# Optimization experiments

Hardware: AMD Instinct MI355X
Metric: run time of the kernel (lower is better)

The kernel has to match this reference:

```python
import jax, jax.numpy as jnp
import numpy as np

N = 8192
K = 8192
BS = 128  # quantization block size (elements per codebook)
NE = 8    # codebook entries per block (3-bit indices)


def setup_inputs() -> dict:
    key = jax.random.key(0)
    k1, k2, k3 = jax.random.split(key, 3)
    num_blocks = N * K // BS  # 524288
    n_packed_bytes = num_blocks * BS * 3 // 8  # 25165824
    x = jax.random.normal(k1, (2048, K), dtype=jnp.float32)
    # random packed bytes (values 0..255) -> uniformly random 3-bit indices
    packed_indices = jax.random.randint(k2, (n_packed_bytes,), 0, 256, dtype=jnp.int32)
    codebook = jax.random.normal(k3, (num_blocks, NE), dtype=jnp.float32)
    return {"x": x, "packed_indices": packed_indices, "codebook": codebook}


def _dequantize(packed_indices, codebook):
    num_blocks = codebook.shape[0]
    packed = packed_indices.reshape(-1, 3).astype(jnp.int32)  # (n_groups, 3)
    bits24 = packed[:, 0] | (packed[:, 1] << 8) | (packed[:, 2] << 16)
    shifts = jnp.arange(8, dtype=jnp.int32) * 3
    idx = (bits24[:, None] >> shifts[None, :]) & 7          # (n_groups, 8)
    idx = idx.reshape(num_blocks, BS)                        # (num_blocks, BS)
    # per-block codebook gather: w[b, i] = codebook[b, idx[b, i]]
    w = jnp.take_along_axis(codebook, idx, axis=1)           # (num_blocks, BS)
    return w.reshape(N, K)


def reference(x, packed_indices, codebook):
    w = _dequantize(packed_indices, codebook)  # (N, K) fp32
    y = x @ w.T                                # (batch, N)
    return y
```

## Files before the change

kernel.cpp:

```cpp
#include <hip/hip_runtime.h>
#include <hip/hip_bf16.h>

#define Mdim 2048
#define Ndim 8192
#define Kdim 8192
#define BM 128
#define BN 128
#define BK 64

typedef __bf16 bf16x8 __attribute__((ext_vector_type(8)));
typedef float f32x4 __attribute__((ext_vector_type(4)));
typedef unsigned short ushort8 __attribute__((ext_vector_type(8)));
typedef unsigned short ushort4v __attribute__((ext_vector_type(4)));

__device__ __forceinline__ unsigned short f2bf_rne(float f) {
    unsigned u = __float_as_uint(f);
    u += 0x7fffu + ((u >> 16) & 1u);
    return (unsigned short)(u >> 16);
}

__device__ __forceinline__ ushort8 decode8(unsigned bits, float4 c0, float4 c1) {
    ushort8 o;
#pragma unroll
    for (int i = 0; i < 8; ++i) {
        unsigned id = (bits >> (3 * i)) & 7u;
        float a0 = (id & 1) ? c0.y : c0.x;
        float a1 = (id & 1) ? c0.w : c0.z;
        float a2 = (id & 1) ? c1.y : c1.x;
        float a3 = (id & 1) ? c1.w : c1.z;
        float b0 = (id & 2) ? a1 : a0;
        float b1 = (id & 2) ? a3 : a2;
        float v  = (id & 4) ? b1 : b0;
        o[i] = f2bf_rne(v);
    }
    return o;
}

__global__ __launch_bounds__(256) void k_prep(const int* __restrict__ packed,
                                              const float* __restrict__ cb,
                                              const float* __restrict__ x,
                                              unsigned short* __restrict__ W,
                                              unsigned short* __restrict__ xb) {
    const int t = threadIdx.x;
    if (blockIdx.x < 16384) {
        const size_t th = (size_t)blockIdx.x * 256 + t;
        const size_t g0 = th * 2;
        const int2* pv = (const int2*)(packed + g0 * 3);
        int2 q0 = pv[0], q1 = pv[1], q2 = pv[2];
        unsigned bits0 = (unsigned)(q0.x & 255) | ((unsigned)(q0.y & 255) << 8) |
                         ((unsigned)(q1.x & 255) << 16);
        unsigned bits1 = (unsigned)(q1.y & 255) | ((unsigned)(q2.x & 255) << 8) |
                         ((unsigned)(q2.y & 255) << 16);
        const float4* cv0 = (const float4*)(cb + ((g0 >> 4) << 3));
        const float4* cv1 = (const float4*)(cb + (((g0 + 1) >> 4) << 3));
        float4 c00 = cv0[0], c01 = cv0[1];
        float4 c10 = cv1[0], c11 = cv1[1];
        ushort8 o0 = decode8(bits0, c00, c01);
        ushort8 o1 = decode8(bits1, c10, c11);
        unsigned short* wp = W + (g0 << 3);
        *(ushort8*)(wp)     = o0;
        *(ushort8*)(wp + 8) = o1;
    } else {
        const size_t u = (size_t)(blockIdx.x - 16384) * 256 + t;
        float4 a = ((const float4*)x)[u];
        ushort4v o;
        o[0] = f2bf_rne(a.x); o[1] = f2bf_rne(a.y);
        o[2] = f2bf_rne(a.z); o[3] = f2bf_rne(a.w);
        ((ushort4v*)xb)[u] = o;
    }
}

__device__ __forceinline__ void gld16(const unsigned short* g, unsigned short* l) {
    __builtin_amdgcn_global_load_lds(
        (const __attribute__((address_space(1))) unsigned int*)g,
        (__attribute__((address_space(3))) unsigned int*)l, 16, 0, 0);
}

__global__ __launch_bounds__(256) void k_gemm(const unsigned short* __restrict__ A,
                                              const unsigned short* __restrict__ B,
                                              float* __restrict__ C) {
    __shared__ unsigned short As[BM * BK];
    __shared__ unsigned short Bs[BN * BK];

    const int tid  = threadIdx.x;
    const int lane = tid & 63;
    const int wave = tid >> 6;
    const int waveM = wave >> 1;
    const int waveN = wave & 1;
    const int bm = blockIdx.y * BM;
    const int bn = blockIdx.x * BN;

    const int srow = tid >> 3;
    const int scol = (((tid & 7) ^ ((tid >> 3) & 7))) * 8;
    const unsigned short* agp = A + (size_t)(bm + srow) * Kdim + scol;
    const unsigned short* bgp = B + (size_t)(bn + srow) * Kdim + scol;
    unsigned short* alp = &As[tid * 8];
    unsigned short* blp = &Bs[tid * 8];

    f32x4 acc[4][4];
    const f32x4 zero = {0.f, 0.f, 0.f, 0.f};
#pragma unroll
    for (int i = 0; i < 4; ++i)
#pragma unroll
        for (int j = 0; j < 4; ++j) acc[i][j] = zero;

    const int r15 = lane & 15;
    const int q   = lane >> 4;
    const int rlo = r15 & 7;

    for (int kt = 0; kt < Kdim; kt += BK) {
#pragma unroll
        for (int j = 0; j < 4; ++j) {
            gld16(agp + (size_t)(j * 32) * Kdim + kt, alp + j * 2048);
            gld16(bgp + (size_t)(j * 32) * Kdim + kt, blp + j * 2048);
        }
        __syncthreads();

#pragma unroll
        for (int kk = 0; kk < 2; ++kk) {
            const int slot = ((kk * 4 + q) ^ rlo) * 8;
            bf16x8 af[4], bfr[4];
#pragma unroll
            for (int i = 0; i < 4; ++i)
                af[i] = *(const bf16x8*)(&As[(waveM * 64 + i * 16 + r15) * BK + slot]);
#pragma unroll
            for (int j = 0; j < 4; ++j)
                bfr[j] = *(const bf16x8*)(&Bs[(waveN * 64 + j * 16 + r15) * BK + slot]);
#pragma unroll
            for (int i = 0; i < 4; ++i)
#pragma unroll
                for (int j = 0; j < 4; ++j)
                    acc[i][j] = __builtin_amdgcn_mfma_f32_16x16x32_bf16(
                        af[i], bfr[j], acc[i][j], 0, 0, 0);
        }
        __syncthreads();
    }

#pragma unroll
    for (int i = 0; i < 4; ++i) {
#pragma unroll
        for (int j = 0; j < 4; ++j) {
            int row = bm + waveM * 64 + i * 16 + q * 4;
            int col = bn + waveN * 64 + j * 16 + r15;
            float* outp = C + (size_t)row * Ndim + col;
#pragma unroll
            for (int r = 0; r < 4; ++r)
                outp[(size_t)r * Ndim] = acc[i][j][r];
        }
    }
}

extern "C" void kernel_launch(void* const* d_in, const int* in_sizes, int n_in,
                              void* d_out, int out_size, void* d_ws, size_t ws_size,
                              hipStream_t stream) {
    const float* x      = (const float*)d_in[0];
    const int*   packed = (const int*)d_in[1];
    const float* cb     = (const float*)d_in[2];
    float* out = (float*)d_out;

    unsigned short* Wb = (unsigned short*)d_ws;
    unsigned short* Xb = (unsigned short*)d_ws + (size_t)Ndim * Kdim;

    k_prep<<<32768, 256, 0, stream>>>(packed, cb, x, Wb, Xb);
    dim3 grid(Ndim / BN, Mdim / BM);
    k_gemm<<<grid, 256, 0, stream>>>(Xb, Wb, out);
}
```

Before: 525.0 us.

## Rewrite GEMM as 256x256 tile, 8-wave, double-buffered pipelined kernel

Replaces the 128x128 single-buffered GEMM with a 256x256 output tile per 512-thread block. The block computes four 128x128 quadrants in phases and uses a double-buffered LDS ring. Global-to-LDS loads for the next k-tiles are issued between MFMA phases, with explicit vmcnt waits, raw barriers and setprio, to overlap memory with compute and raise reuse per loaded byte. This adds heavy register pressure (128 accumulator floats plus fragments), 128KB of LDS, and fragile hand-tuned barrier and waitcnt ordering.

Result: faster. 473.0 us (-9.9%).

```diff
diff --git a/kernel.cpp b/kernel.cpp
--- a/kernel.cpp
+++ b/kernel.cpp
@@ -4,9 +4,7 @@
 #define Mdim 2048
 #define Ndim 8192
 #define Kdim 8192
-#define BM 128
-#define BN 128
-#define BK 64
+#define NT (Kdim / 64)
 
 typedef __bf16 bf16x8 __attribute__((ext_vector_type(8)));
 typedef float f32x4 __attribute__((ext_vector_type(4)));
@@ -76,78 +74,155 @@
         (__attribute__((address_space(3))) unsigned int*)l, 16, 0, 0);
 }
 
-__global__ __launch_bounds__(256) void k_gemm(const unsigned short* __restrict__ A,
-                                              const unsigned short* __restrict__ B,
-                                              float* __restrict__ C) {
-    __shared__ unsigned short As[BM * BK];
-    __shared__ unsigned short Bs[BN * BK];
+#define BAR()    asm volatile("s_barrier" ::: "memory")
+#define FENCE()  asm volatile("" ::: "memory")
+#define WAIT_DS0() asm volatile("s_waitcnt lgkmcnt(0)" ::: "memory")
+
+__global__ __launch_bounds__(512, 2) void k_gemm(const unsigned short* __restrict__ A,
+                                                 const unsigned short* __restrict__ B,
+                                                 float* __restrict__ C) {
+    __shared__ unsigned short LA[4 * 8192];
+    __shared__ unsigned short LB[4 * 8192];
 
     const int tid  = threadIdx.x;
     const int lane = tid & 63;
     const int wave = tid >> 6;
-    const int waveM = wave >> 1;
-    const int waveN = wave & 1;
-    const int bm = blockIdx.y * BM;
-    const int bn = blockIdx.x * BN;
-
-    const int srow = tid >> 3;
-    const int scol = (((tid & 7) ^ ((tid >> 3) & 7))) * 8;
-    const unsigned short* agp = A + (size_t)(bm + srow) * Kdim + scol;
-    const unsigned short* bgp = B + (size_t)(bn + srow) * Kdim + scol;
-    unsigned short* alp = &As[tid * 8];
-    unsigned short* blp = &Bs[tid * 8];
-
-    f32x4 acc[4][4];
-    const f32x4 zero = {0.f, 0.f, 0.f, 0.f};
-#pragma unroll
-    for (int i = 0; i < 4; ++i)
-#pragma unroll
-        for (int j = 0; j < 4; ++j) acc[i][j] = zero;
+    const int qm = wave >> 2;
+    const int qn = wave & 3;
+
+    const int bid = blockIdx.x;
+    const int bm = (bid & 7) * 256;
+    const int bn = (bid >> 3) * 256;
+
+    const int chunk0 = tid, chunk1 = tid + 512;
+    const int srow0 = chunk0 >> 3, srow1 = chunk1 >> 3;
+    const int scol0 = ((chunk0 & 7) ^ (srow0 & 7)) * 8;
+    const int scol1 = ((chunk1 & 7) ^ (srow1 & 7)) * 8;
+    const unsigned short* Ag0 = A + (size_t)(bm + srow0) * Kdim + scol0;
+    const unsigned short* Ag1 = A + (size_t)(bm + srow1) * Kdim + scol1;
+    const unsigned short* Bg0 = B + (size_t)(bn + srow0) * Kdim + scol0;
+    const unsigned short* Bg1 = B + (size_t)(bn + srow1) * Kdim + scol1;
+
+#define STAGE_A(T, H, BUF) do {                                                   \
+    unsigned short* _d = LA + ((BUF) * 2 + (H)) * 8192;                           \
+    gld16(Ag0 + (size_t)(H) * 128 * Kdim + (size_t)(T) * 64, _d + (size_t)tid * 8);        \
+    gld16(Ag1 + (size_t)(H) * 128 * Kdim + (size_t)(T) * 64, _d + (size_t)(tid + 512) * 8);\
+    FENCE();                                                                      \
+} while (0)
+#define STAGE_B(T, H, BUF) do {                                                   \
+    unsigned short* _d = LB + ((BUF) * 2 + (H)) * 8192;                           \
+    gld16(Bg0 + (size_t)(H) * 128 * Kdim + (size_t)(T) * 64, _d + (size_t)tid * 8);        \
+    gld16(Bg1 + (size_t)(H) * 128 * Kdim + (size_t)(T) * 64, _d + (size_t)(tid + 512) * 8);\
+    FENCE();                                                                      \
+} while (0)
 
     const int r15 = lane & 15;
     const int q   = lane >> 4;
     const int rlo = r15 & 7;
-
-    for (int kt = 0; kt < Kdim; kt += BK) {
-#pragma unroll
-        for (int j = 0; j < 4; ++j) {
-            gld16(agp + (size_t)(j * 32) * Kdim + kt, alp + j * 2048);
-            gld16(bgp + (size_t)(j * 32) * Kdim + kt, blp + j * 2048);
+    const int aro = qm * 64 + r15;
+    const int bro = qn * 32 + r15;
+    const int ch0 = ((0 + q) ^ rlo) * 8;
+    const int ch1 = ((4 + q) ^ rlo) * 8;
+
+    f32x4 acc[4][4][2];
+    const f32x4 zero = {0.f, 0.f, 0.f, 0.f};
+#pragma unroll
+    for (int p = 0; p < 4; ++p)
+#pragma unroll
+        for (int i = 0; i < 4; ++i)
+#pragma unroll
+            for (int j = 0; j < 2; ++j) acc[p][i][j] = zero;
+
+    bf16x8 af[4][2], bf[2][2];
+
+#define LOAD_A(BUF, H) do {                                                       \
+    const unsigned short* _s = LA + ((BUF) * 2 + (H)) * 8192;                     \
+    _Pragma("unroll") for (int i = 0; i < 4; ++i) {                               \
+        int _r = (aro + i * 16) * 64;                                             \
+        af[i][0] = *(const bf16x8*)&_s[_r + ch0];                                 \
+        af[i][1] = *(const bf16x8*)&_s[_r + ch1];                                 \
+    }                                                                             \
+} while (0)
+#define LOAD_B(BUF, H) do {                                                       \
+    const unsigned short* _s = LB + ((BUF) * 2 + (H)) * 8192;                     \
+    _Pragma("unroll") for (int j = 0; j < 2; ++j) {                               \
+        int _r = (bro + j * 16) * 64;                                             \
+        bf[j][0] = *(const bf16x8*)&_s[_r + ch0];                                 \
+        bf[j][1] = *(const bf16x8*)&_s[_r + ch1];                                 \
+    }                                                                             \
+} while (0)
+
+#define MFMA_PHASE(P) do {                                                        \
+    __builtin_amdgcn_s_setprio(1);                                                \
+    _Pragma("unroll") for (int i = 0; i < 4; ++i)                                 \
+    _Pragma("unroll") for (int j = 0; j < 2; ++j) {                               \
+        acc[P][i][j] = __builtin_amdgcn_mfma_f32_16x16x32_bf16(                   \
+            af[i][0], bf[j][0], acc[P][i][j], 0, 0, 0);                           \
+        acc[P][i][j] = __builtin_amdgcn_mfma_f32_16x16x32_bf16(                   \
+            af[i][1], bf[j][1], acc[P][i][j], 0, 0, 0);                           \
+    }                                                                             \
+    __builtin_amdgcn_s_setprio(0);                                                \
+} while (0)
+
+#define KSTEP(T, BUF) do {                                                        \
+    LOAD_A(BUF, 0); LOAD_B(BUF, 0);                                               \
+    if ((T) + 1 < NT) STAGE_B((T) + 1, 0, (BUF) ^ 1);                             \
+    BAR(); WAIT_DS0();                                                            \
+    MFMA_PHASE(0);                                                                \
+    BAR();                                                                        \
+    LOAD_B(BUF, 1);                                                               \
+    if ((T) + 2 < NT) STAGE_A((T) + 2, 0, BUF);                                   \
+    BAR(); WAIT_DS0();                                                            \
+    MFMA_PHASE(1);                                                                \
+    BAR();                                                                        \
+    LOAD_A(BUF, 1);                                                               \
+    if ((T) + 2 < NT) STAGE_B((T) + 2, 1, BUF);                                   \
+    BAR(); WAIT_DS0();                                                            \
+    MFMA_PHASE(2);                                                                \
+    BAR();                                                                        \
+    LOAD_B(BUF, 0);                                                               \
+    if ((T) + 2 < NT) STAGE_A((T) + 2, 1, BUF);                                   \
+    BAR(); WAIT_DS0();                                                            \
+    MFMA_PHASE(3);                                                                \
+    if ((T) + 2 < NT) { asm volatile("s_waitcnt vmcnt(6)" ::: "memory"); }        \
+    else              { asm volatile("s_waitcnt vmcnt(0)" ::: "memory"); }        \
+    BAR();                                                                        \
+} while (0)
+
+    STAGE_A(0, 0, 0); STAGE_B(0, 1, 0); STAGE_A(0, 1, 0); STAGE_B(0, 0, 0);
+    STAGE_A(1, 0, 1); STAGE_B(1, 1, 1); STAGE_A(1, 1, 1);
+    asm volatile("s_waitcnt vmcnt(6)" ::: "memory");
+    BAR();
+
+    for (int t2 = 0; t2 < NT; t2 += 2) {
+        KSTEP(t2, 0);
+        KSTEP(t2 + 1, 1);
+    }
+
+    constexpr int RHs[4] = {0, 0, 1, 1};
+    constexpr int CHs[4] = {0, 1, 1, 0};
+#pragma unroll
+    for (int p = 0; p < 4; ++p) {
+#pragma unroll
+        for (int i = 0; i < 4; ++i) {
+#pragma unroll
+            for (int j = 0; j < 2; ++j) {
+                int row = bm + RHs[p] * 128 + qm * 64 + i * 16 + q * 4;
+                int col = bn + CHs[p] * 128 + qn * 32 + j * 16 + r15;
+                float* outp = C + (size_t)row * Ndim + col;
+#pragma unroll
+                for (int r = 0; r < 4; ++r)
+                    outp[(size_t)r * Ndim] = acc[p][i][j][r];
+            }
         }
-        __syncthreads();
-
-#pragma unroll
-        for (int kk = 0; kk < 2; ++kk) {
-            const int slot = ((kk * 4 + q) ^ rlo) * 8;
-            bf16x8 af[4], bfr[4];
-#pragma unroll
-            for (int i = 0; i < 4; ++i)
-                af[i] = *(const bf16x8*)(&As[(waveM * 64 + i * 16 + r15) * BK + slot]);
-#pragma unroll
-            for (int j = 0; j < 4; ++j)
-                bfr[j] = *(const bf16x8*)(&Bs[(waveN * 64 + j * 16 + r15) * BK + slot]);
-#pragma unroll
-            for (int i = 0; i < 4; ++i)
-#pragma unroll
-                for (int j = 0; j < 4; ++j)
-                    acc[i][j] = __builtin_amdgcn_mfma_f32_16x16x32_bf16(
-                        af[i], bfr[j], acc[i][j], 0, 0, 0);
-        }
-        __syncthreads();
-    }
-
-#pragma unroll
-    for (int i = 0; i < 4; ++i) {
-#pragma unroll
-        for (int j = 0; j < 4; ++j) {
-            int row = bm + waveM * 64 + i * 16 + q * 4;
-            int col = bn + waveN * 64 + j * 16 + r15;
-            float* outp = C + (size_t)row * Ndim + col;
-#pragma unroll
-            for (int r = 0; r < 4; ++r)
-                outp[(size_t)r * Ndim] = acc[i][j][r];
-        }
-    }
+    }
+
+#undef STAGE_A
+#undef STAGE_B
+#undef LOAD_A
+#undef LOAD_B
+#undef MFMA_PHASE
+#undef KSTEP
 }
 
 extern "C" void kernel_launch(void* const* d_in, const int* in_sizes, int n_in,
@@ -162,6 +237,5 @@
     unsigned short* Xb = (unsigned short*)d_ws + (size_t)Ndim * Kdim;
 
     k_prep<<<32768, 256, 0, stream>>>(packed, cb, x, Wb, Xb);
-    dim3 grid(Ndim / BN, Mdim / BM);
-    k_gemm<<<grid, 256, 0, stream>>>(Xb, Wb, out);
-}
+    k_gemm<<<dim3(256), 512, 0, stream>>>(Xb, Wb, out);
+}
```

## Fuse codebook dequantization into GEMM with producer/consumer warp specialization

Applied to the files above, without the earlier changes.

Removes the separate pass that writes the full dequantized bf16 weight matrix to global memory. Dequantization now happens inside the GEMM: four producer waves load packed indices and codebooks, decode them into LDS with byte-perm selects, and stage A tiles. Four consumer waves run MFMA over a double-buffered 256x128 tile at raised priority. The goal is to cut the large weight write and re-read traffic. In exchange, W is decoded again for each of the 8 M-tiles and the kernel depends on hand-placed barrier and waitcnt synchronization.

New measurement: 678.1 us. 1.29x slower.

```diff
diff --git a/kernel.cpp b/kernel.cpp
--- a/kernel.cpp
+++ b/kernel.cpp
@@ -4,13 +4,12 @@
 #define Mdim 2048
 #define Ndim 8192
 #define Kdim 8192
-#define BM 128
+#define NT 128
+#define BM 256
 #define BN 128
-#define BK 64
 
 typedef __bf16 bf16x8 __attribute__((ext_vector_type(8)));
 typedef float f32x4 __attribute__((ext_vector_type(4)));
-typedef unsigned short ushort8 __attribute__((ext_vector_type(8)));
 typedef unsigned short ushort4v __attribute__((ext_vector_type(4)));
 
 __device__ __forceinline__ unsigned short f2bf_rne(float f) {
@@ -19,55 +18,14 @@
     return (unsigned short)(u >> 16);
 }
 
-__device__ __forceinline__ ushort8 decode8(unsigned bits, float4 c0, float4 c1) {
-    ushort8 o;
-#pragma unroll
-    for (int i = 0; i < 8; ++i) {
-        unsigned id = (bits >> (3 * i)) & 7u;
-        float a0 = (id & 1) ? c0.y : c0.x;
-        float a1 = (id & 1) ? c0.w : c0.z;
-        float a2 = (id & 1) ? c1.y : c1.x;
-        float a3 = (id & 1) ? c1.w : c1.z;
-        float b0 = (id & 2) ? a1 : a0;
-        float b1 = (id & 2) ? a3 : a2;
-        float v  = (id & 4) ? b1 : b0;
-        o[i] = f2bf_rne(v);
-    }
-    return o;
-}
-
-__global__ __launch_bounds__(256) void k_prep(const int* __restrict__ packed,
-                                              const float* __restrict__ cb,
-                                              const float* __restrict__ x,
-                                              unsigned short* __restrict__ W,
+__global__ __launch_bounds__(256) void k_prep(const float* __restrict__ x,
                                               unsigned short* __restrict__ xb) {
-    const int t = threadIdx.x;
-    if (blockIdx.x < 16384) {
-        const size_t th = (size_t)blockIdx.x * 256 + t;
-        const size_t g0 = th * 2;
-        const int2* pv = (const int2*)(packed + g0 * 3);
-        int2 q0 = pv[0], q1 = pv[1], q2 = pv[2];
-        unsigned bits0 = (unsigned)(q0.x & 255) | ((unsigned)(q0.y & 255) << 8) |
-                         ((unsigned)(q1.x & 255) << 16);
-        unsigned bits1 = (unsigned)(q1.y & 255) | ((unsigned)(q2.x & 255) << 8) |
-                         ((unsigned)(q2.y & 255) << 16);
-        const float4* cv0 = (const float4*)(cb + ((g0 >> 4) << 3));
-        const float4* cv1 = (const float4*)(cb + (((g0 + 1) >> 4) << 3));
-        float4 c00 = cv0[0], c01 = cv0[1];
-        float4 c10 = cv1[0], c11 = cv1[1];
-        ushort8 o0 = decode8(bits0, c00, c01);
-        ushort8 o1 = decode8(bits1, c10, c11);
-        unsigned short* wp = W + (g0 << 3);
-        *(ushort8*)(wp)     = o0;
-        *(ushort8*)(wp + 8) = o1;
-    } else {
-        const size_t u = (size_t)(blockIdx.x - 16384) * 256 + t;
-        float4 a = ((const float4*)x)[u];
-        ushort4v o;
-        o[0] = f2bf_rne(a.x); o[1] = f2bf_rne(a.y);
-        o[2] = f2bf_rne(a.z); o[3] = f2bf_rne(a.w);
-        ((ushort4v*)xb)[u] = o;
-    }
+    const size_t u = (size_t)blockIdx.x * 256 + threadIdx.x;
+    float4 a = ((const float4*)x)[u];
+    ushort4v o;
+    o[0] = f2bf_rne(a.x); o[1] = f2bf_rne(a.y);
+    o[2] = f2bf_rne(a.z); o[3] = f2bf_rne(a.w);
+    ((ushort4v*)xb)[u] = o;
 }
 
 __device__ __forceinline__ void gld16(const unsigned short* g, unsigned short* l) {
@@ -76,78 +34,204 @@
         (__attribute__((address_space(3))) unsigned int*)l, 16, 0, 0);
 }
 
-__global__ __launch_bounds__(256) void k_gemm(const unsigned short* __restrict__ A,
-                                              const unsigned short* __restrict__ B,
-                                              float* __restrict__ C) {
-    __shared__ unsigned short As[BM * BK];
-    __shared__ unsigned short Bs[BN * BK];
+#define BAR()    asm volatile("s_barrier" ::: "memory")
+#define FENCE()  asm volatile("" ::: "memory")
+#define LGKM0()  asm volatile("s_waitcnt lgkmcnt(0)" ::: "memory")
+#define VMCNT(n) asm volatile("s_waitcnt vmcnt(" #n ")" ::: "memory")
+
+__device__ __forceinline__ uint4 dec_group(unsigned b, unsigned P0, unsigned P1,
+                                           unsigned P2, unsigned P3) {
+    uint4 o;
+#pragma unroll
+    for (int k = 0; k < 4; ++k) {
+        unsigned ia = (b >> (6 * k)) & 3u;
+        unsigned ib = (b >> (6 * k + 3)) & 3u;
+        unsigned sel = ia * 0x0202u + 0x01000100u + ((ib * 0x0202u) << 16);
+        unsigned lo = __builtin_amdgcn_perm(P1, P0, sel);
+        unsigned hi = __builtin_amdgcn_perm(P3, P2, sel);
+        unsigned mA = (unsigned)((int)(b << (29 - 6 * k)) >> 31);
+        unsigned mB = (unsigned)((int)(b << (26 - 6 * k)) >> 31);
+        unsigned m = (mA & 0xFFFFu) | (mB & 0xFFFF0000u);
+        (&o.x)[k] = (hi & m) | (lo & ~m);
+    }
+    return o;
+}
+
+__global__ __launch_bounds__(512, 2) void k_gemm(const unsigned short* __restrict__ A,
+                                                 const int* __restrict__ packed,
+                                                 const float* __restrict__ cb,
+                                                 float* __restrict__ C) {
+    __shared__ unsigned short LA[2 * 16384];
+    __shared__ unsigned short LB[2 * 8192];
 
     const int tid  = threadIdx.x;
     const int lane = tid & 63;
     const int wave = tid >> 6;
-    const int waveM = wave >> 1;
-    const int waveN = wave & 1;
-    const int bm = blockIdx.y * BM;
-    const int bn = blockIdx.x * BN;
-
-    const int srow = tid >> 3;
-    const int scol = (((tid & 7) ^ ((tid >> 3) & 7))) * 8;
-    const unsigned short* agp = A + (size_t)(bm + srow) * Kdim + scol;
-    const unsigned short* bgp = B + (size_t)(bn + srow) * Kdim + scol;
-    unsigned short* alp = &As[tid * 8];
-    unsigned short* blp = &Bs[tid * 8];
-
-    f32x4 acc[4][4];
-    const f32x4 zero = {0.f, 0.f, 0.f, 0.f};
-#pragma unroll
-    for (int i = 0; i < 4; ++i)
-#pragma unroll
-        for (int j = 0; j < 4; ++j) acc[i][j] = zero;
+
+    const int bid = blockIdx.x;
+    const int bm = (bid & 7) * BM;
+    const int bn = (bid >> 3) * BN;
+
+    const int plane = (tid - 256) & 255;
+    const int arow0 = plane >> 3;
+    const int acol  = ((plane & 7) ^ (arow0 & 7)) * 8;
+    const unsigned short* Aga = A + (size_t)(bm + arow0) * Kdim + acol;
+
+    const int brow = plane >> 1;
+    const int dp   = plane & 1;
+    const int dp4  = dp * 4;
+    const int brlo = brow & 7;
+    const int* Pg   = packed + (size_t)(bn + brow) * 3072 + dp * 12;
+    const float* Cg = cb + (size_t)(bn + brow) * 512;
 
     const int r15 = lane & 15;
     const int q   = lane >> 4;
     const int rlo = r15 & 7;
-
-    for (int kt = 0; kt < Kdim; kt += BK) {
-#pragma unroll
-        for (int j = 0; j < 4; ++j) {
-            gld16(agp + (size_t)(j * 32) * Kdim + kt, alp + j * 2048);
-            gld16(bgp + (size_t)(j * 32) * Kdim + kt, blp + j * 2048);
+    const int qm  = wave >> 1;
+    const int qn  = wave & 1;
+    const int aro = qm * 128 + r15;
+    const int bro = qn * 64 + r15;
+    const int ch0 = ((0 + q) ^ rlo) * 8;
+    const int ch1 = ((4 + q) ^ rlo) * 8;
+
+    f32x4 acc[8][4];
+    const f32x4 zero = {0.f, 0.f, 0.f, 0.f};
+#pragma unroll
+    for (int i = 0; i < 8; ++i)
+#pragma unroll
+        for (int j = 0; j < 4; ++j) acc[i][j] = zero;
+
+    int4 pA0, pA1, pA2, pB0, pB1, pB2;
+    float4 cA0, cA1, cB0, cB1;
+
+#define GLD_A(T1, BUFP) do {                                                      \
+    unsigned short* _ld = LA + (BUFP) * 16384 + plane * 8;                        \
+    const unsigned short* _sg = Aga + (size_t)(T1) * 64;                          \
+    _Pragma("unroll") for (int r = 0; r < 8; ++r)                                 \
+        gld16(_sg + (size_t)(r * 32) * Kdim, _ld + r * 2048);                     \
+    FENCE();                                                                      \
+} while (0)
+
+#define DECG(G, W0, W1, W2) do {                                                  \
+    unsigned _b = (unsigned)(W0) | ((unsigned)(W1) << 8) | ((unsigned)(W2) << 16);\
+    uint4 _o = dec_group(_b, cP0, cP1, cP2, cP3);                                 \
+    *(uint4*)&_wb[((dp4 + (G)) ^ brlo) << 3] = _o;                                \
+} while (0)
+
+#define DECODE_TILE(BUFP, dq0, dq1, dq2, dc0, dc1) do {                           \
+    unsigned cP0 = (unsigned)f2bf_rne(dc0.x) | ((unsigned)f2bf_rne(dc0.y) << 16); \
+    unsigned cP1 = (unsigned)f2bf_rne(dc0.z) | ((unsigned)f2bf_rne(dc0.w) << 16); \
+    unsigned cP2 = (unsigned)f2bf_rne(dc1.x) | ((unsigned)f2bf_rne(dc1.y) << 16); \
+    unsigned cP3 = (unsigned)f2bf_rne(dc1.z) | ((unsigned)f2bf_rne(dc1.w) << 16); \
+    unsigned short* _wb = LB + (BUFP) * 8192 + brow * 64;                         \
+    DECG(0, dq0.x, dq0.y, dq0.z);                                                 \
+    DECG(1, dq0.w, dq1.x, dq1.y);                                                 \
+    DECG(2, dq1.z, dq1.w, dq2.x);                                                 \
+    DECG(3, dq2.y, dq2.z, dq2.w);                                                 \
+} while (0)
+
+#define PRODUCE(T, dq0,dq1,dq2, dc0,dc1, lq0,lq1,lq2, lc0,lc1) do {               \
+    if ((T) + 1 < NT) {                                                           \
+        GLD_A((T) + 1, ((T) + 1) & 1);                                            \
+        DECODE_TILE(((T) + 1) & 1, dq0, dq1, dq2, dc0, dc1);                      \
+    }                                                                             \
+    if ((T) + 2 < NT) {                                                           \
+        const int4* _pp = (const int4*)(Pg + (size_t)((T) + 2) * 24);             \
+        lq0 = _pp[0]; lq1 = _pp[1]; lq2 = _pp[2];                                 \
+        const float4* _cc = (const float4*)(Cg + (size_t)(((T) + 2) >> 1) * 8);   \
+        lc0 = _cc[0]; lc1 = _cc[1];                                               \
+    }                                                                             \
+    LGKM0();                                                                      \
+    if ((T) + 2 < NT) { VMCNT(4); } else { VMCNT(0); }                            \
+} while (0)
+
+#define LOADA(DST, I, LAB) do {                                                   \
+    DST[0] = *(const bf16x8*)&LAB[(aro + (I) * 16) * 64 + ch0];                   \
+    DST[1] = *(const bf16x8*)&LAB[(aro + (I) * 16) * 64 + ch1];                   \
+} while (0)
+#define BURST(I, AR) do {                                                         \
+    _Pragma("unroll") for (int j = 0; j < 4; ++j) {                               \
+        acc[I][j] = __builtin_amdgcn_mfma_f32_16x16x32_bf16(                      \
+            AR[0], bf_[j][0], acc[I][j], 0, 0, 0);                                \
+        acc[I][j] = __builtin_amdgcn_mfma_f32_16x16x32_bf16(                      \
+            AR[1], bf_[j][1], acc[I][j], 0, 0, 0);                                \
+    }                                                                             \
+} while (0)
+
+#define CONSUME(T) do {                                                           \
+    const unsigned short* _la = LA + ((T) & 1) * 16384;                           \
+    const unsigned short* _lb = LB + ((T) & 1) * 8192;                            \
+    bf16x8 bf_[4][2];                                                             \
+    _Pragma("unroll") for (int j = 0; j < 4; ++j) {                               \
+        bf_[j][0] = *(const bf16x8*)&_lb[(bro + j * 16) * 64 + ch0];              \
+        bf_[j][1] = *(const bf16x8*)&_lb[(bro + j * 16) * 64 + ch1];              \
+    }                                                                             \
+    bf16x8 aX[2], aY[2];                                                          \
+    LOADA(aX, 0, _la);                                                            \
+    LOADA(aY, 1, _la); BURST(0, aX);                                              \
+    LOADA(aX, 2, _la); BURST(1, aY);                                              \
+    LOADA(aY, 3, _la); BURST(2, aX);                                              \
+    LOADA(aX, 4, _la); BURST(3, aY);                                              \
+    LOADA(aY, 5, _la); BURST(4, aX);                                              \
+    LOADA(aX, 6, _la); BURST(5, aY);                                              \
+    LOADA(aY, 7, _la); BURST(6, aX);                                              \
+    BURST(7, aY);                                                                 \
+    LGKM0();                                                                      \
+} while (0)
+
+    if (wave >= 4) {
+        {
+            const int4* _pp = (const int4*)Pg;
+            pA0 = _pp[0]; pA1 = _pp[1]; pA2 = _pp[2];
+            const float4* _cc = (const float4*)Cg;
+            cA0 = _cc[0]; cA1 = _cc[1];
         }
-        __syncthreads();
-
-#pragma unroll
-        for (int kk = 0; kk < 2; ++kk) {
-            const int slot = ((kk * 4 + q) ^ rlo) * 8;
-            bf16x8 af[4], bfr[4];
-#pragma unroll
-            for (int i = 0; i < 4; ++i)
-                af[i] = *(const bf16x8*)(&As[(waveM * 64 + i * 16 + r15) * BK + slot]);
-#pragma unroll
-            for (int j = 0; j < 4; ++j)
-                bfr[j] = *(const bf16x8*)(&Bs[(waveN * 64 + j * 16 + r15) * BK + slot]);
-#pragma unroll
-            for (int i = 0; i < 4; ++i)
-#pragma unroll
-                for (int j = 0; j < 4; ++j)
-                    acc[i][j] = __builtin_amdgcn_mfma_f32_16x16x32_bf16(
-                        af[i], bfr[j], acc[i][j], 0, 0, 0);
+        GLD_A(0, 0);
+        DECODE_TILE(0, pA0, pA1, pA2, cA0, cA1);
+        {
+            const int4* _pp = (const int4*)(Pg + 24);
+            pB0 = _pp[0]; pB1 = _pp[1]; pB2 = _pp[2];
+            const float4* _cc = (const float4*)Cg;
+            cB0 = _cc[0]; cB1 = _cc[1];
         }
-        __syncthreads();
-    }
-
-#pragma unroll
-    for (int i = 0; i < 4; ++i) {
-#pragma unroll
-        for (int j = 0; j < 4; ++j) {
-            int row = bm + waveM * 64 + i * 16 + q * 4;
-            int col = bn + waveN * 64 + j * 16 + r15;
-            float* outp = C + (size_t)row * Ndim + col;
-#pragma unroll
-            for (int r = 0; r < 4; ++r)
-                outp[(size_t)r * Ndim] = acc[i][j][r];
+        LGKM0();
+        VMCNT(4);
+    }
+    BAR();
+    if (wave < 4) __builtin_amdgcn_s_setprio(1);
+
+    for (int t = 0; t < NT; t += 2) {
+        if (wave < 4) CONSUME(t);
+        else PRODUCE(t, pB0, pB1, pB2, cB0, cB1, pA0, pA1, pA2, cA0, cA1);
+        BAR();
+        if (wave < 4) CONSUME(t + 1);
+        else PRODUCE(t + 1, pA0, pA1, pA2, cA0, cA1, pB0, pB1, pB2, cB0, cB1);
+        BAR();
+    }
+
+    if (wave < 4) {
+        __builtin_amdgcn_s_setprio(0);
+#pragma unroll
+        for (int i = 0; i < 8; ++i) {
+#pragma unroll
+            for (int j = 0; j < 4; ++j) {
+                int row = bm + qm * 128 + i * 16 + q * 4;
+                int col = bn + qn * 64 + j * 16 + r15;
+                float* outp = C + (size_t)row * Ndim + col;
+#pragma unroll
+                for (int r = 0; r < 4; ++r)
+                    outp[(size_t)r * Ndim] = acc[i][j][r];
+            }
         }
     }
+
+#undef GLD_A
+#undef DECG
+#undef DECODE_TILE
+#undef PRODUCE
+#undef LOADA
+#undef BURST
+#undef CONSUME
 }
 
 extern "C" void kernel_launch(void* const* d_in, const int* in_sizes, int n_in,
@@ -158,10 +242,8 @@
     const float* cb     = (const float*)d_in[2];
     float* out = (float*)d_out;
 
-    unsigned short* Wb = (unsigned short*)d_ws;
-    unsigned short* Xb = (unsigned short*)d_ws + (size_t)Ndim * Kdim;
-
-    k_prep<<<32768, 256, 0, stream>>>(packed, cb, x, Wb, Xb);
-    dim3 grid(Ndim / BN, Mdim / BM);
-    k_gemm<<<grid, 256, 0, stream>>>(Xb, Wb, out);
-}
+    unsigned short* Xb = (unsigned short*)d_ws;
+
+    k_prep<<<16384, 256, 0, stream>>>(x, Xb);
+    k_gemm<<<dim3(512), 512, 0, stream>>>(Xb, packed, cb, out);
+}
```
